# Optimization experiments

Hardware: AMD Instinct MI355X
Metric: run time of the kernel (lower is better)

The kernel has to match this reference:

```python
import jax, jax.numpy as jnp
import numpy as np

H = 1024      # hidden_dim
V = 50257     # vocab_size
E = 512       # embedding_dim
PAD = 0       # padding_idx
B = 128       # batch
S = 512       # src_len


def setup_inputs() -> dict:
    key = jax.random.key(0)
    ks = jax.random.split(key, 16)
    sc = 0.02
    emb_table = jax.random.normal(ks[0], (V, E), jnp.float32) * sc
    emb_table = emb_table.at[PAD].set(0.0)  # padding_idx row is zero
    return {
        "decoder_input": jax.random.randint(ks[1], (B,), 0, V),
        "decoder_hidden": jax.random.normal(ks[2], (1, B, H), jnp.float32),
        "encoder_outputs": jax.random.normal(ks[3], (B, S, 2 * H), jnp.float32),
        "emb_table": emb_table,
        "W_ah": jax.random.normal(ks[4], (H, H), jnp.float32) * sc,
        "b_ah": jnp.zeros((H,), jnp.float32),
        "W_ae": jax.random.normal(ks[5], (H, 2 * H), jnp.float32) * sc,
        "b_ae": jnp.zeros((H,), jnp.float32),
        "w_score": jax.random.normal(ks[6], (H,), jnp.float32) * sc,
        "W_ih": jax.random.normal(ks[7], (3 * H, E + 2 * H), jnp.float32) * sc,
        "W_hh": jax.random.normal(ks[8], (3 * H, H), jnp.float32) * sc,
        "b_ih": jnp.zeros((3 * H,), jnp.float32),
        "b_hh": jnp.zeros((3 * H,), jnp.float32),
        "W_out": jax.random.normal(ks[9], (V, H), jnp.float32) * sc,
        "b_out": jnp.zeros((V,), jnp.float32),
    }


def reference(decoder_input, decoder_hidden, encoder_outputs, emb_table,
              W_ah, b_ah, W_ae, b_ae, w_score, W_ih, W_hh, b_ih, b_hh,
              W_out, b_out):
    h = decoder_hidden[0]                                  # [B,H]
    emb = emb_table[decoder_input]                         # [B,E]

    # Bahdanau attention
    ah = h @ W_ah.T + b_ah                                 # [B,H]
    ae = jnp.einsum('bsd,hd->bsh', encoder_outputs, W_ae) + b_ae  # [B,S,H]
    scores = jnp.tanh(ah[:, None, :] + ae) @ w_score       # [B,S]
    attn = jax.nn.softmax(scores, axis=1)                  # [B,S]
    ctx = jnp.einsum('bs,bsd->bd', attn, encoder_outputs)  # [B,2H]

    # GRU single step (PyTorch gate layout: r, z, n)
    x = jnp.concatenate([emb, ctx], axis=1)                # [B,E+2H]
    gx = x @ W_ih.T + b_ih                                 # [B,3H]
    gh = h @ W_hh.T + b_hh                                 # [B,3H]
    r = jax.nn.sigmoid(gx[:, :H] + gh[:, :H])
    z = jax.nn.sigmoid(gx[:, H:2 * H] + gh[:, H:2 * H])
    n = jnp.tanh(gx[:, 2 * H:] + r * gh[:, 2 * H:])
    h_new = (1.0 - z) * n + z * h                          # [B,H]

    out = h_new @ W_out.T + b_out                          # [B,V]
    return out[:, None, :], h_new[None]                    # [B,1,V], [1,B,H]
```

## Files before the change

### kernel.cpp

```cpp
#include <hip/hip_runtime.h>
#include <hip/hip_bf16.h>

#define DEVI __device__ __forceinline__

typedef short bf16x8 __attribute__((ext_vector_type(8)));
typedef float f32x4  __attribute__((ext_vector_type(4)));

static constexpr int Bb   = 128;
static constexpr int Ss   = 512;
static constexpr int Hh   = 1024;
static constexpr int Ee   = 512;
static constexpr int Vv   = 50257;
static constexpr int TWOH = 2048;

DEVI short f2bf(float f){ __hip_bfloat16 h = __float2bfloat16(f); return *reinterpret_cast<short*>(&h); }
DEVI float bf2f(short s){ __hip_bfloat16 h = *reinterpret_cast<__hip_bfloat16*>(&s); return __bfloat162float(h); }

DEVI float tanh_fast(float x){
  float e = __expf(2.0f*x);
  return 1.0f - 2.0f/(e + 1.0f);
}

DEVI bf16x8 pack8(f32x4 a, f32x4 b){
  bf16x8 v;
  v[0]=f2bf(a[0]); v[1]=f2bf(a[1]); v[2]=f2bf(a[2]); v[3]=f2bf(a[3]);
  v[4]=f2bf(b[0]); v[5]=f2bf(b[1]); v[6]=f2bf(b[2]); v[7]=f2bf(b[3]);
  return v;
}

DEVI void gld_lds16(const void* g, void* l){
  __builtin_amdgcn_global_load_lds((const __attribute__((address_space(1))) void*)g,
                                   (__attribute__((address_space(3))) void*)l, 16, 0, 0);
}

DEVI f32x4 mfma16(bf16x8 a, bf16x8 b, f32x4 c){
  return __builtin_amdgcn_mfma_f32_16x16x32_bf16(a, b, c, 0, 0, 0);
}

__global__ void k_prep(const float* __restrict__ wae, short* __restrict__ waeb,
                       const float* __restrict__ h, short* __restrict__ hb,
                       const int* __restrict__ dec_in, const float* __restrict__ emb,
                       short* __restrict__ xb)
{
  const int total_wae = Hh*TWOH;
  const int total_h   = Bb*Hh;
  const int total_emb = Bb*Ee;
  const int total = total_wae + total_h + total_emb;
  for (int i = blockIdx.x*blockDim.x + threadIdx.x; i < total; i += gridDim.x*blockDim.x){
    if (i < total_wae) waeb[i] = f2bf(wae[i]);
    else if (i < total_wae + total_h){ int j = i - total_wae; hb[j] = f2bf(h[j]); }
    else {
      int j = i - total_wae - total_h;
      int b = j >> 9, e = j & 511;
      xb[b*2560 + e] = f2bf(emb[(size_t)dec_in[b]*Ee + e]);
    }
  }
}

__launch_bounds__(512)
__global__ void k_scores_fuse(const float* __restrict__ enc, short* __restrict__ encb,
                              const short* __restrict__ waeb,
                              const float* __restrict__ ahb, const float* __restrict__ b_ah,
                              const float* __restrict__ b_ae, const float* __restrict__ wsc,
                              float* __restrict__ scores)
{
  __shared__ __align__(16) char LDSB[131072];
  const int q  = blockIdx.x;
  const int xcd = q & 7, sl = q >> 3;
  const int rt = xcd*32 + (sl>>2), nb = sl & 3;
  const int tid = threadIdx.x, wid = tid>>6, lane = tid&63;
  const int wr = wid>>2, wc = wid&3;
  const int srow = lane>>3, l7 = lane&7;
  const int lo = lane&15, hi4 = lane>>4;
  const int swk = (l7 ^ srow)*8;

  const float* Ag = enc  + (size_t)rt*256*TWOH + (size_t)(wid*8+srow)*TWOH + swk;
  const short* Bg = waeb + (size_t)nb*256*TWOH + (size_t)(wid*8+srow)*TWOH + swk;
  short*       Eg = encb + (size_t)rt*256*TWOH + (size_t)(wid*8+srow)*TWOH + swk;
  const bool we = (nb == 0) && (encb != nullptr);

  char* AWc = LDSB + wid*1024 + lane*16;
  char* BW  = LDSB + 65536 + wid*1024;
  const char* AR = LDSB + (wr*128 + lo)*128;
  const char* BR = LDSB + 65536 + (wc*64 + lo)*128;
  const int sw0 = (hi4*16) ^ (l7<<4);
  const int sw1 = (64 + hi4*16) ^ (l7<<4);

  f32x4 acc[8][4] = {};
  f32x4 pa[4][2];

  auto STB = [&](int buf, int kt){
    #pragma unroll
    for (int rnd=0; rnd<4; ++rnd)
      gld_lds16(Bg + (size_t)rnd*64*TWOH + kt*64, BW + buf*32768 + rnd*8192);
  };
  auto PREFA = [&](int kt){
    #pragma unroll
    for (int rnd=0; rnd<4; ++rnd){
      const float* p = Ag + (size_t)rnd*64*TWOH + kt*64;
      pa[rnd][0] = *(const f32x4*)p; pa[rnd][1] = *(const f32x4*)(p+4);
    }
  };
  auto COMMITA = [&](int buf){
    #pragma unroll
    for (int rnd=0; rnd<4; ++rnd)
      *(bf16x8*)(AWc + buf*32768 + rnd*8192) = pack8(pa[rnd][0], pa[rnd][1]);
  };
  auto STOREE = [&](int kt){
    #pragma unroll
    for (int rnd=0; rnd<4; ++rnd)
      *(bf16x8*)(Eg + (size_t)rnd*64*TWOH + kt*64) = pack8(pa[rnd][0], pa[rnd][1]);
  };

  PREFA(0); STB(0,0); COMMITA(0);
  if (we) STOREE(0);
  PREFA(1);
  __syncthreads();

  for (int t = 0; t < 32; ++t){
    const int cur = t&1, nxt = cur^1;
    const int aO = cur*32768, bO = cur*32768;
    bf16x8 af[4], bq[4];

    if (t<31){ STB(nxt, t+1); PREFA(t+1); }
    #pragma unroll
    for (int j=0;j<4;++j) bq[j] = *(const bf16x8*)(BR + bO + j*2048 + sw0);
    #pragma unroll
    for (int i=0;i<4;++i) af[i] = *(const bf16x8*)(AR + aO + i*2048 + sw0);
    __builtin_amdgcn_s_setprio(1);
    #pragma unroll
    for (int i=0;i<4;++i)
      #pragma unroll
      for (int j=0;j<4;++j)
        acc[i][j] = mfma16(af[i], bq[j], acc[i][j]);
    __builtin_amdgcn_s_setprio(0);
    #pragma unroll
    for (int i=0;i<4;++i) af[i] = *(const bf16x8*)(AR + aO + (4+i)*2048 + sw0);
    __builtin_amdgcn_s_setprio(1);
    #pragma unroll
    for (int i=0;i<4;++i)
      #pragma unroll
      for (int j=0;j<4;++j)
        acc[4+i][j] = mfma16(af[i], bq[j], acc[4+i][j]);
    __builtin_amdgcn_s_setprio(0);

    if (t<31){ COMMITA(nxt); if (we) STOREE(t+1); }
    #pragma unroll
    for (int j=0;j<4;++j) bq[j] = *(const bf16x8*)(BR + bO + j*2048 + sw1);
    #pragma unroll
    for (int i=0;i<4;++i) af[i] = *(const bf16x8*)(AR + aO + i*2048 + sw1);
    __builtin_amdgcn_s_setprio(1);
    #pragma unroll
    for (int i=0;i<4;++i)
      #pragma unroll
      for (int j=0;j<4;++j)
        acc[i][j] = mfma16(af[i], bq[j], acc[i][j]);
    __builtin_amdgcn_s_setprio(0);
    #pragma unroll
    for (int i=0;i<4;++i) af[i] = *(const bf16x8*)(AR + aO + (4+i)*2048 + sw1);
    __builtin_amdgcn_s_setprio(1);
    #pragma unroll
    for (int i=0;i<4;++i)
      #pragma unroll
      for (int j=0;j<4;++j)
        acc[4+i][j] = mfma16(af[i], bq[j], acc[4+i][j]);
    __builtin_amdgcn_s_setprio(0);

    asm volatile("s_waitcnt lgkmcnt(0)" ::: "memory");
    __builtin_amdgcn_s_barrier();
    __builtin_amdgcn_sched_barrier(0);
  }
  const int b = rt >> 1;
  float w4[4], t4[4];
  #pragma unroll
  for (int j=0;j<4;++j){
    int n = nb*256 + wc*64 + j*16 + lo;
    w4[j] = wsc[n];
    t4[j] = ahb[b*Hh + n] + b_ah[n] + b_ae[n];
  }
  #pragma unroll
  for (int i=0;i<8;++i){
    #pragma unroll
    for (int q2=0;q2<4;++q2){
      int m = rt*256 + wr*128 + i*16 + hi4*4 + q2;
      float s = 0.f;
      #pragma unroll
      for (int j=0;j<4;++j) s += tanh_fast(t4[j] + acc[i][j][q2]) * w4[j];
      s += __shfl_xor(s,1); s += __shfl_xor(s,2); s += __shfl_xor(s,4); s += __shfl_xor(s,8);
      if (lo == 0) atomicAdd(&scores[m], s);
    }
  }
}

template<int MODE>
__launch_bounds__(256)
__global__ void k_gemm128(const short* __restrict__ A, int lda,
                          const float* __restrict__ B0, const float* __restrict__ B1,
                          float* __restrict__ O0, float* __restrict__ O1,
                          const float* __restrict__ bias, int kiters)
{
  __shared__ __align__(16) short As[2][128*64];
  __shared__ __align__(16) short Bs[2][128*64];
  const int nb = blockIdx.x;
  const int tid = threadIdx.x, wid = tid>>6, lane = tid&63;
  const int wr = wid>>1, wc = wid&1;
  const int srow = lane>>3, l7 = lane&7;
  const int swk = (l7 ^ srow) * 8;

  const float* Bt; int noff; float* Ot; int ostride;
  if constexpr (MODE==0){
    if (nb < 8){ Bt = B0; noff = 0;    Ot = O0; ostride = Hh;   }
    else       { Bt = B1; noff = 1024; Ot = O1; ostride = 3*Hh; }
  } else if constexpr (MODE==1){ Bt = B0; noff = 0; Ot = O0; ostride = 3*Hh; }
  else { Bt = B0; noff = 0; Ot = O0; ostride = Vv; }

  f32x4 acc[4][4] = {};
  f32x4 pb0[4], pb1[4];

  auto stageA = [&](int s, int kt){
    #pragma unroll
    for (int i=0;i<4;++i){
      int c = wid*4+i, row = c*8+srow;
      gld_lds16(A + (size_t)row*lda + kt*64 + swk, (char*)As[s] + c*1024);
    }
  };
  auto prefB = [&](int kt){
    #pragma unroll
    for (int i=0;i<4;++i){
      int row = (wid*4+i)*8+srow;
      int n = nb*128 + row - noff;
      if constexpr (MODE==2) n = (n > Vv-1) ? (Vv-1) : n;
      const float* bp = Bt + (size_t)n*lda + kt*64 + l7*8;
      pb0[i] = *(const f32x4*)bp; pb1[i] = *(const f32x4*)(bp+4);
    }
  };
  auto commitB = [&](int s){
    #pragma unroll
    for (int i=0;i<4;++i){
      int row = (wid*4+i)*8+srow;
      *(bf16x8*)((char*)Bs[s] + row*128 + ((l7^srow)<<4)) = pack8(pb0[i], pb1[i]);
    }
  };

  const int kt0 = blockIdx.y * kiters, kend = kt0 + kiters;
  stageA(0, kt0); prefB(kt0); commitB(0);
  __syncthreads();

  int cur = 0;
  for (int kt = kt0; kt < kend; ++kt){
    if (kt+1 < kend){ stageA(cur^1, kt+1); prefB(kt+1); }
    #pragma unroll
    for (int kk=0;kk<2;++kk){
      bf16x8 af[4], bq[4];
      const int sw = (kk*64 + (lane>>4)*16) ^ (l7<<4);
      #pragma unroll
      for (int i=0;i<4;++i) af[i] = *(const bf16x8*)((const char*)As[cur] + (wr*64+i*16+(lane&15))*128 + sw);
      #pragma unroll
      for (int j=0;j<4;++j) bq[j] = *(const bf16x8*)((const char*)Bs[cur] + (wc*64+j*16+(lane&15))*128 + sw);
      #pragma unroll
      for (int i=0;i<4;++i)
        #pragma unroll
        for (int j=0;j<4;++j)
          acc[i][j] = mfma16(af[i], bq[j], acc[i][j]);
    }
    if (kt+1 < kend) commitB(cur^1);
    __syncthreads();
    cur ^= 1;
  }
  const int lo = lane&15, hi = lane>>4;
  #pragma unroll
  for (int i=0;i<4;++i){
    #pragma unroll
    for (int j=0;j<4;++j){
      int n = nb*128 + wc*64 + j*16 + lo - noff;
      #pragma unroll
      for (int q=0;q<4;++q){
        int m = wr*64 + i*16 + hi*4 + q;
        float v = acc[i][j][q];
        if constexpr (MODE==2){
          if (n < Vv) O0[(size_t)m*Vv + n] = v + bias[n];
        } else {
          atomicAdd(&Ot[(size_t)m*ostride + n], v);
        }
      }
    }
  }
}

__global__ void k_softmax(const float* __restrict__ scores, float* __restrict__ attn)
{
  __shared__ float red[512];
  const int b = blockIdx.x, tid = threadIdx.x;
  float v = scores[b*Ss + tid];
  red[tid] = v; __syncthreads();
  for (int off=256; off>0; off>>=1){ if (tid<off) red[tid] = fmaxf(red[tid], red[tid+off]); __syncthreads(); }
  float mx = red[0]; __syncthreads();
  float e = __expf(v - mx);
  red[tid] = e; __syncthreads();
  for (int off=256; off>0; off>>=1){ if (tid<off) red[tid] += red[tid+off]; __syncthreads(); }
  attn[b*Ss + tid] = e / red[0];
}

__global__ void k_ctx_bf16(const short* __restrict__ encb, const float* __restrict__ attn,
                           float* __restrict__ ctxp)
{
  __shared__ float a[128];
  const int bid = blockIdx.x, b = bid>>2, ch = bid&3, tid = threadIdx.x;
  if (tid < 128) a[tid] = attn[b*Ss + ch*128 + tid];
  __syncthreads();
  const short* e0 = encb + (size_t)(b*Ss + ch*128)*TWOH + tid*8;
  float s[8] = {};
  for (int r=0; r<128; ++r){
    bf16x8 v = *(const bf16x8*)(e0 + (size_t)r*TWOH);
    float w = a[r];
    #pragma unroll
    for (int j=0;j<8;++j) s[j] += w * bf2f(v[j]);
  }
  float* o = ctxp + (size_t)ch*Bb*TWOH + (size_t)b*TWOH + tid*8;
  #pragma unroll
  for (int j=0;j<8;++j) o[j] = s[j];
}

__global__ void k_ctxfin(const float* __restrict__ ctxp, short* __restrict__ xb)
{
  const int g = blockIdx.x*256 + threadIdx.x;
  const int b = g >> 11, col = g & 2047;
  const int N = Bb*TWOH;
  float v = ctxp[g] + ctxp[N+g] + ctxp[2*N+g] + ctxp[3*N+g];
  xb[b*2560 + 512 + col] = f2bf(v);
}

__global__ void k_ctx_f32(const float* __restrict__ enc, const float* __restrict__ attn,
                          short* __restrict__ xb)
{
  __shared__ float a[512];
  const int ch = blockIdx.x, b = blockIdx.y, tid = threadIdx.x;
  a[tid]     = attn[b*Ss + tid];
  a[tid+256] = attn[b*Ss + tid + 256];
  __syncthreads();
  const float* e0 = enc + (size_t)b*Ss*TWOH + ch*256 + tid;
  float s0=0.f, s1=0.f, s2=0.f, s3=0.f;
  for (int s=0; s<512; s+=4){
    s0 += a[s]   * e0[(size_t)(s  )*TWOH];
    s1 += a[s+1] * e0[(size_t)(s+1)*TWOH];
    s2 += a[s+2] * e0[(size_t)(s+2)*TWOH];
    s3 += a[s+3] * e0[(size_t)(s+3)*TWOH];
  }
  xb[b*2560 + 512 + ch*256 + tid] = f2bf(s0+s1+s2+s3);
}

__global__ void k_gates(const float* __restrict__ gx, const float* __restrict__ gh,
                        const float* __restrict__ b_ih, const float* __restrict__ b_hh,
                        const float* __restrict__ h, float* __restrict__ hnew_out,
                        short* __restrict__ hnewb)
{
  const int gid = blockIdx.x*256 + threadIdx.x;
  const int b = gid >> 10, j = gid & 1023;
  float xr = gx[b*3072 + j]        + b_ih[j];
  float xz = gx[b*3072 + 1024 + j] + b_ih[1024+j];
  float xn = gx[b*3072 + 2048 + j] + b_ih[2048+j];
  float hr = gh[b*3072 + j]        + b_hh[j];
  float hz = gh[b*3072 + 1024 + j] + b_hh[1024+j];
  float hn = gh[b*3072 + 2048 + j] + b_hh[2048+j];
  float r = 1.f/(1.f + __expf(-(xr+hr)));
  float z = 1.f/(1.f + __expf(-(xz+hz)));
  float n = tanhf(xn + r*hn);
  float hv = (1.f - z)*n + z*h[b*Hh + j];
  hnew_out[gid] = hv;
  hnewb[gid] = f2bf(hv);
}

extern "C" void kernel_launch(void* const* d_in, const int* in_sizes, int n_in,
                              void* d_out, int out_size, void* d_ws, size_t ws_size,
                              hipStream_t stream)
{
  const int*   dec   = (const int*)  d_in[0];
  const float* h     = (const float*)d_in[1];
  const float* enc   = (const float*)d_in[2];
  const float* emb   = (const float*)d_in[3];
  const float* W_ah  = (const float*)d_in[4];
  const float* b_ah  = (const float*)d_in[5];
  const float* W_ae  = (const float*)d_in[6];
  const float* b_ae  = (const float*)d_in[7];
  const float* wsc   = (const float*)d_in[8];
  const float* W_ih  = (const float*)d_in[9];
  const float* W_hh  = (const float*)d_in[10];
  const float* b_ih  = (const float*)d_in[11];
  const float* b_hh  = (const float*)d_in[12];
  const float* W_out = (const float*)d_in[13];
  const float* b_out = (const float*)d_in[14];
  float* out = (float*)d_out;
  float* hnew_out = out + (size_t)Bb*Vv;

  char* w = (char*)d_ws;
  float* scores = (float*)w;  w += (size_t)65536*4;
  float* ahb    = (float*)w;  w += (size_t)131072*4;
  float* ghb    = (float*)w;  w += (size_t)393216*4;
  float* gxb    = (float*)w;  w += (size_t)393216*4;
  size_t zero_bytes = (size_t)(w - (char*)d_ws);
  float* attn   = (float*)w;  w += (size_t)65536*4;
  short* waeb   = (short*)w;  w += (size_t)2097152*2;
  short* xb     = (short*)w;  w += (size_t)128*2560*2;
  short* hb     = (short*)w;  w += (size_t)131072*2;
  short* hnb    = (short*)w;  w += (size_t)131072*2;
  float* ctxp   = (float*)w;  w += (size_t)4*Bb*TWOH*4;
  short* encb   = (short*)w;  w += (size_t)65536*2048*2;
  const bool big = ((size_t)(w - (char*)d_ws) <= ws_size);

  hipMemsetAsync(d_ws, 0, zero_bytes, stream);
  k_prep<<<4096, 256, 0, stream>>>(W_ae, waeb, h, hb, dec, emb, xb);
  k_gemm128<0><<<dim3(32,2), 256, 0, stream>>>(hb, 1024, W_ah, W_hh, ahb, ghb, nullptr, 8);
  k_scores_fuse<<<1024, 512, 0, stream>>>(enc, big ? encb : nullptr, waeb,
                                          ahb, b_ah, b_ae, wsc, scores);
  k_softmax<<<128, 512, 0, stream>>>(scores, attn);
  if (big){
    k_ctx_bf16<<<512, 256, 0, stream>>>(encb, attn, ctxp);
    k_ctxfin<<<1024, 256, 0, stream>>>(ctxp, xb);
  } else {
    k_ctx_f32<<<dim3(8,128), 256, 0, stream>>>(enc, attn, xb);
  }
  k_gemm128<1><<<dim3(24,4), 256, 0, stream>>>(xb, 2560, W_ih, nullptr, gxb, nullptr, nullptr, 10);
  k_gates<<<512, 256, 0, stream>>>(gxb, ghb, b_ih, b_hh, h, hnew_out, hnb);
  k_gemm128<2><<<dim3(393,1), 256, 0, stream>>>(hnb, 1024, W_out, nullptr, out, nullptr, b_out, 16);
}
```

Baseline: 566.1 us.

## Deepen A-operand prefetch to two tiles ahead with explicit vmcnt waits

Restructures the attention-energy GEMM main loop so the fp32 encoder tile loads are issued two k-steps ahead into alternating register sets (paA/paB), with the loop manually unrolled by two to keep register indexing static. Explicit vmcnt waits replace the implicit full drain, so loads for the tile after next stay in flight across the barrier. This is meant to hide global-memory latency on the streamed encoder operand. In exchange it holds twice the prefetch registers, which may hurt occupancy or cause spills, and it relies on hand-counted vmcnt values being correct.

```diff
diff --git a/kernel.cpp b/kernel.cpp
--- a/kernel.cpp
+++ b/kernel.cpp
@@ -87,42 +87,46 @@
   const int sw1 = (64 + hi4*16) ^ (l7<<4);
 
   f32x4 acc[8][4] = {};
-  f32x4 pa[4][2];
+  f32x4 paA[4][2], paB[4][2];
 
   auto STB = [&](int buf, int kt){
     #pragma unroll
     for (int rnd=0; rnd<4; ++rnd)
       gld_lds16(Bg + (size_t)rnd*64*TWOH + kt*64, BW + buf*32768 + rnd*8192);
   };
-  auto PREFA = [&](int kt){
+  auto PREFA = [&](int kt, f32x4 (&pa)[4][2]){
     #pragma unroll
     for (int rnd=0; rnd<4; ++rnd){
       const float* p = Ag + (size_t)rnd*64*TWOH + kt*64;
       pa[rnd][0] = *(const f32x4*)p; pa[rnd][1] = *(const f32x4*)(p+4);
     }
   };
-  auto COMMITA = [&](int buf){
+  auto COMMITA = [&](int buf, f32x4 (&pa)[4][2]){
     #pragma unroll
     for (int rnd=0; rnd<4; ++rnd)
       *(bf16x8*)(AWc + buf*32768 + rnd*8192) = pack8(pa[rnd][0], pa[rnd][1]);
   };
-  auto STOREE = [&](int kt){
+  auto STOREE = [&](int kt, f32x4 (&pa)[4][2]){
     #pragma unroll
     for (int rnd=0; rnd<4; ++rnd)
       *(bf16x8*)(Eg + (size_t)rnd*64*TWOH + kt*64) = pack8(pa[rnd][0], pa[rnd][1]);
   };
 
-  PREFA(0); STB(0,0); COMMITA(0);
-  if (we) STOREE(0);
-  PREFA(1);
-  __syncthreads();
-
-  for (int t = 0; t < 32; ++t){
+  PREFA(0, paA); STB(0,0); COMMITA(0, paA);
+  if (we) STOREE(0, paA);
+  PREFA(1, paA);
+  asm volatile("s_waitcnt vmcnt(8)" ::: "memory");
+  asm volatile("s_waitcnt lgkmcnt(0)" ::: "memory");
+  __builtin_amdgcn_s_barrier();
+  __builtin_amdgcn_sched_barrier(0);
+
+  auto TILE = [&](int t, f32x4 (&paC)[4][2], f32x4 (&paN)[4][2]){
     const int cur = t&1, nxt = cur^1;
     const int aO = cur*32768, bO = cur*32768;
     bf16x8 af[4], bq[4];
 
-    if (t<31){ STB(nxt, t+1); PREFA(t+1); }
+    if (t<31) STB(nxt, t+1);
+    __builtin_amdgcn_sched_barrier(0);
     #pragma unroll
     for (int j=0;j<4;++j) bq[j] = *(const bf16x8*)(BR + bO + j*2048 + sw0);
     #pragma unroll
@@ -144,7 +148,11 @@
         acc[4+i][j] = mfma16(af[i], bq[j], acc[4+i][j]);
     __builtin_amdgcn_s_setprio(0);
 
-    if (t<31){ COMMITA(nxt); if (we) STOREE(t+1); }
+    if (t<31){
+      COMMITA(nxt, paC);
+      if (we) STOREE(t+1, paC);
+    }
+    if (t<30) PREFA(t+2, paN);
     #pragma unroll
     for (int j=0;j<4;++j) bq[j] = *(const bf16x8*)(BR + bO + j*2048 + sw1);
     #pragma unroll
@@ -166,10 +174,21 @@
         acc[4+i][j] = mfma16(af[i], bq[j], acc[4+i][j]);
     __builtin_amdgcn_s_setprio(0);
 
-    asm volatile("s_waitcnt lgkmcnt(0)" ::: "memory");
-    __builtin_amdgcn_s_barrier();
-    __builtin_amdgcn_sched_barrier(0);
-  }
+    if (t<30)       asm volatile("s_waitcnt vmcnt(8)" ::: "memory");
+    else if (t==30) asm volatile("s_waitcnt vmcnt(0)" ::: "memory");
+    if (t<31){
+      asm volatile("s_waitcnt lgkmcnt(0)" ::: "memory");
+      __builtin_amdgcn_s_barrier();
+      __builtin_amdgcn_sched_barrier(0);
+    }
+  };
+
+  #pragma unroll 1
+  for (int tt = 0; tt < 16; ++tt){
+    TILE(2*tt,   paA, paB);
+    TILE(2*tt+1, paB, paA);
+  }
+
   const int b = rt >> 1;
   float w4[4], t4[4];
   #pragma unroll
```

Result: slower. 969.2 us (+71.2%).
